# Kernel tuning notes

Measured on AMD Instinct MI355X. Metric: run time of the kernel, lower is better.

The kernel has to match this reference:

```python
import jax, jax.numpy as jnp
import numpy as np

N_AGENTS = 32
STATE_DIM = 6 * N_AGENTS      # 192
CONTROL_DIM = 3 * N_AGENTS    # 96
HIDDEN = 100
NEWTON_ITERS = 40

# Index maps from the cvxpy objective:
#   p[u_x_r]^T u[u_idx] + p[u_y_r]^T u[2*u_idx] + p[u_z_r]^T u[3*u_idx]
_u_idx = np.arange(N_AGENTS)
P_IDX = np.concatenate([3 * np.arange(1, N_AGENTS + 1),
                        4 * np.arange(1, N_AGENTS + 1),
                        5 * np.arange(1, N_AGENTS + 1)])
U_IDX = np.concatenate([_u_idx, 2 * _u_idx, 3 * _u_idx])


def _p_net(t, z, W1, b1, W2, b2, W3, b3):
    # DefaultPNet: MLP on concat([t, z]) with tanh hiddens (hidden_dim=100)
    x = jnp.concatenate([t, z], axis=-1)          # [B, 1+STATE_DIM]
    h = jnp.tanh(x @ W1 + b1)
    h = jnp.tanh(h @ W2 + b2)
    return h @ W3 + b3                            # [B, STATE_DIM]


def _solve_qp(q):
    # min_u q^T u + 0.5||u||^2 + 0.25||u||^4  (unconstrained, strictly convex)
    # Stationarity: q + (1+||u||^2) u = 0 => u = -q/(1+s), s = ||u||^2
    # => s (1+s)^2 = ||q||^2 ; solve scalar cubic per row via Newton.
    r = jnp.sum(q * q, axis=-1)                   # [B]
    s0 = jnp.cbrt(r)                              # good init: s ~ r^(1/3) for large r

    def step(s, _):
        one = 1.0 + s
        f = s * one * one - r
        fp = one * one + 2.0 * s * one
        return jnp.maximum(s - f / fp, 0.0), None

    s, _ = jax.lax.scan(step, s0, None, length=NEWTON_ITERS)
    return -q / (1.0 + s)[:, None]                # [B, CONTROL_DIM]


def setup_inputs() -> dict:
    key = jax.random.key(0)
    ks = jax.random.split(key, 8)
    B = 131072
    in_dim = 1 + STATE_DIM
    sc1 = 1.0 / np.sqrt(in_dim)
    sc2 = 1.0 / np.sqrt(HIDDEN)
    return {
        "z": jax.random.normal(ks[0], (B, STATE_DIM), jnp.float32),
        "t": jax.random.uniform(ks[1], (B, 1), jnp.float32),
        "W1": jax.random.normal(ks[2], (in_dim, HIDDEN), jnp.float32) * sc1,
        "b1": jnp.zeros((HIDDEN,), jnp.float32),
        "W2": jax.random.normal(ks[3], (HIDDEN, HIDDEN), jnp.float32) * sc2,
        "b2": jnp.zeros((HIDDEN,), jnp.float32),
        "W3": jax.random.normal(ks[4], (HIDDEN, STATE_DIM), jnp.float32) * sc2,
        "b3": jnp.zeros((STATE_DIM,), jnp.float32),
    }


def reference(z, t, W1, b1, W2, b2, W3, b3):
    p = _p_net(t, z, W1, b1, W2, b2, W3, b3)      # [B, STATE_DIM]
    # Accumulate linear coefficients onto u (indices overlap, so scatter-add)
    q = jnp.zeros((p.shape[0], CONTROL_DIM), p.dtype).at[:, U_IDX].add(p[:, P_IDX])
    return _solve_qp(q)                            # ustar [B, CONTROL_DIM]
```

## Files before the change

kernel.cpp:

```cpp
#include <hip/hip_runtime.h>
#include <hip/hip_bf16.h>


typedef __attribute__((ext_vector_type(8))) short short8;
typedef __attribute__((ext_vector_type(4))) float f32x4;

__device__ __forceinline__ unsigned short f2bf(float f) {
  unsigned u = __float_as_uint(f);
  u += 0x7fffu + ((u >> 16) & 1u);
  return (unsigned short)(u >> 16);
}
__device__ __forceinline__ float tanh_fast(float x) {
  float ax = fabsf(x);
  float e = __builtin_amdgcn_exp2f(ax * -2.88539008177792681f);
  float r = (1.f - e) * __builtin_amdgcn_rcpf(1.f + e);
  return copysignf(r, x);
}
__device__ __forceinline__ short8 pack_bf8(f32x4 a, f32x4 b) {
  union { short8 s; __hip_bfloat162 h[4]; } u;
  u.h[0] = __float22bfloat162_rn(make_float2(a[0], a[1]));
  u.h[1] = __float22bfloat162_rn(make_float2(a[2], a[3]));
  u.h[2] = __float22bfloat162_rn(make_float2(b[0], b[1]));
  u.h[3] = __float22bfloat162_rn(make_float2(b[2], b[3]));
  return u.s;
}
__device__ __forceinline__ unsigned pk2u(float lo, float hi) {
  union { __hip_bfloat162 h; unsigned u; } x;
  x.h = __float22bfloat162_rn(make_float2(lo, hi));
  return x.u;
}

__global__ void cvx_prep(const float* __restrict__ W1, const float* __restrict__ b1,
                         const float* __restrict__ W2, const float* __restrict__ b2,
                         const float* __restrict__ W3, const float* __restrict__ b3,
                         short* __restrict__ pw) {
  int idx = blockIdx.x * 256 + threadIdx.x;

  if (idx < 21504) {
    int kt = idx / 3584, rem = idx % 3584;
    int nt = rem / 512, e = rem % 512;
    int lane = e >> 3, j = e & 7;
    int k = kt * 32 + (lane >> 4) * 8 + j;
    int n = nt * 16 + (lane & 15);
    float wv = (n < 100) ? W1[(k + 1) * 100 + n] : 0.f;
    pw[(kt * 7 + nt) * 512 + e] = (short)f2bf(wv);
    return;
  }
  idx -= 21504;
  if (idx < 14336) {
    int kt = idx / 3584, rem = idx % 3584;
    int nt = rem / 512, e = rem % 512;
    int lane = e >> 3, j = e & 7;
    int k = kt * 32 + (lane >> 4) * 8 + j;
    int n = nt * 16 + (lane & 15);
    float wv = (k < 100 && n < 100) ? W2[k * 100 + n] : 0.f;
    pw[21504 + (kt * 7 + nt) * 512 + e] = (short)f2bf(wv);
    return;
  }
  idx -= 14336;
  if (idx < 12288) {
    int kt = idx / 3072, rem = idx % 3072;
    int nt = rem / 512, e = rem % 512;
    int lane = e >> 3, j = e & 7;
    int k = kt * 32 + (lane >> 4) * 8 + j;
    int u = nt * 16 + (lane & 15);
    float wv = 0.f;
    if (k < 100) {
      const float* wr = W3 + k * 192;
      if (u <= 31) wv += wr[3 * u + 3];
      if ((u & 1) == 0 && u <= 62) wv += wr[2 * u + 4];
      if (u % 3 == 0 && u <= 93) wv += wr[(5 * u) / 3 + 5];
    }
    pw[35840 + (kt * 6 + nt) * 512 + e] = (short)f2bf(wv);
    return;
  }
  idx -= 12288;
  float* cb = (float*)(pw + 48128);
  if (idx < 112) { cb[idx] = (idx < 100) ? W1[idx] : 0.f; return; }
  idx -= 112;
  if (idx < 112) { cb[112 + idx] = (idx < 100) ? b1[idx] : 0.f; return; }
  idx -= 112;
  if (idx < 112) { cb[224 + idx] = (idx < 100) ? b2[idx] : 0.f; return; }
  idx -= 112;
  if (idx < 96) {
    int u = idx;
    float v = 0.f;
    if (u <= 31) v += b3[3 * u + 3];
    if ((u & 1) == 0 && u <= 62) v += b3[2 * u + 4];
    if (u % 3 == 0 && u <= 93) v += b3[(5 * u) / 3 + 5];
    cb[336 + u] = v;
  }
}

__global__ __launch_bounds__(512, 2) void cvx_main(
    const float* __restrict__ zin, const float* __restrict__ tin,
    const short* __restrict__ pw, float* __restrict__ out) {
  __shared__ __align__(16) short wbuf[48128];
  __shared__ __align__(16) float cbl[448];

  const int tid = threadIdx.x;
  const int wid = tid >> 6;
  const int lane = tid & 63;
  const int l15 = lane & 15;
  const int qd = lane >> 4;
  const int lo_src = ((lane & 16) << 1) + l15;
  const int hi_src = lo_src + 16;
  const bool selA = lane < 32;

  for (int f = wid; f < 94; f += 8) {
    const short* g = pw + f * 512 + lane * 8;
    __builtin_amdgcn_global_load_lds(
        (const __attribute__((address_space(1))) void*)g,
        (__attribute__((address_space(3))) void*)&wbuf[f * 512], 16, 0, 0);
  }
  if (tid < 448) cbl[tid] = ((const float*)(pw + 48128))[tid];

  const int row0 = blockIdx.x * 512 + wid * 32;

  short8 XB[2][6];
  float tc0, tc1;
#pragma unroll
  for (int bt = 0; bt < 2; bt++) {
    const float* zr = zin + (size_t)(row0 + bt * 16 + l15) * 192 + qd * 8;
#pragma unroll
    for (int kt = 0; kt < 6; kt++) {
      f32x4 a = *(const f32x4*)(zr + kt * 32);
      f32x4 b = *(const f32x4*)(zr + kt * 32 + 4);
      XB[bt][kt] = pack_bf8(a, b);
    }
  }
  tc0 = tin[row0 + l15];
  tc1 = tin[row0 + 16 + l15];

  __syncthreads();

  auto buildHB = [&](const unsigned (&pkb)[7][2], int kt) -> short8 {
    union { short8 s; unsigned u[4]; } hb;
    if (kt < 3) {
      unsigned a0 = (unsigned)__shfl((int)pkb[2 * kt][0], lo_src);
      unsigned b0 = (unsigned)__shfl((int)pkb[2 * kt + 1][0], lo_src);
      unsigned a1 = (unsigned)__shfl((int)pkb[2 * kt][1], lo_src);
      unsigned b1_ = (unsigned)__shfl((int)pkb[2 * kt + 1][1], lo_src);
      unsigned a2 = (unsigned)__shfl((int)pkb[2 * kt][0], hi_src);
      unsigned b2_ = (unsigned)__shfl((int)pkb[2 * kt + 1][0], hi_src);
      unsigned a3 = (unsigned)__shfl((int)pkb[2 * kt][1], hi_src);
      unsigned b3_ = (unsigned)__shfl((int)pkb[2 * kt + 1][1], hi_src);
      hb.u[0] = selA ? a0 : b0;
      hb.u[1] = selA ? a1 : b1_;
      hb.u[2] = selA ? a2 : b2_;
      hb.u[3] = selA ? a3 : b3_;
    } else {
      hb.u[0] = (unsigned)__shfl((int)pkb[6][0], lo_src);
      hb.u[1] = (unsigned)__shfl((int)pkb[6][1], lo_src);
      hb.u[2] = (unsigned)__shfl((int)pkb[6][0], hi_src);
      hb.u[3] = (unsigned)__shfl((int)pkb[6][1], hi_src);
    }
    return hb.s;
  };

  short8 XN[2][6];
  float tn0, tn1;

#pragma unroll 1
  for (int ii = 0; ii < 2; ++ii) {
    const int rb = row0 + ii * 256;

    f32x4 acc[2][7];
#pragma unroll
    for (int nt = 0; nt < 7; nt++) {
      f32x4 zzz = {0.f, 0.f, 0.f, 0.f};
      acc[0][nt] = zzz; acc[1][nt] = zzz;
    }

    f32x4 sg[2][2][2];
    const float* zb = zin + (size_t)(row0 + 256 + l15) * 192 + qd * 8;

    if (ii == 0) {
#pragma unroll
      for (int bt = 0; bt < 2; bt++)
#pragma unroll
        for (int kp = 0; kp < 2; kp++) {
          sg[bt][kp][0] = *(const f32x4*)(zb + bt * 3072 + kp * 32);
          sg[bt][kp][1] = *(const f32x4*)(zb + bt * 3072 + kp * 32 + 4);
        }
      __builtin_amdgcn_sched_barrier(0);
    }

#pragma unroll
    for (int kt = 0; kt < 2; kt++)
#pragma unroll
      for (int nt = 0; nt < 7; nt++) {
        short8 wf = *(const short8*)&wbuf[(kt * 7 + nt) * 512 + lane * 8];
        acc[0][nt] = __builtin_amdgcn_mfma_f32_16x16x32_bf16(wf, XB[0][kt], acc[0][nt], 0, 0, 0);
        acc[1][nt] = __builtin_amdgcn_mfma_f32_16x16x32_bf16(wf, XB[1][kt], acc[1][nt], 0, 0, 0);
      }

    if (ii == 0) {
#pragma unroll
      for (int bt = 0; bt < 2; bt++)
#pragma unroll
        for (int kp = 0; kp < 2; kp++)
          XN[bt][kp] = pack_bf8(sg[bt][kp][0], sg[bt][kp][1]);
#pragma unroll
      for (int bt = 0; bt < 2; bt++)
#pragma unroll
        for (int kp = 0; kp < 2; kp++) {
          sg[bt][kp][0] = *(const f32x4*)(zb + bt * 3072 + (2 + kp) * 32);
          sg[bt][kp][1] = *(const f32x4*)(zb + bt * 3072 + (2 + kp) * 32 + 4);
        }
      __builtin_amdgcn_sched_barrier(0);
    }

#pragma unroll
    for (int kt = 2; kt < 4; kt++)
#pragma unroll
      for (int nt = 0; nt < 7; nt++) {
        short8 wf = *(const short8*)&wbuf[(kt * 7 + nt) * 512 + lane * 8];
        acc[0][nt] = __builtin_amdgcn_mfma_f32_16x16x32_bf16(wf, XB[0][kt], acc[0][nt], 0, 0, 0);
        acc[1][nt] = __builtin_amdgcn_mfma_f32_16x16x32_bf16(wf, XB[1][kt], acc[1][nt], 0, 0, 0);
      }

    if (ii == 0) {
#pragma unroll
      for (int bt = 0; bt < 2; bt++)
#pragma unroll
        for (int kp = 0; kp < 2; kp++)
          XN[bt][2 + kp] = pack_bf8(sg[bt][kp][0], sg[bt][kp][1]);
#pragma unroll
      for (int bt = 0; bt < 2; bt++)
#pragma unroll
        for (int kp = 0; kp < 2; kp++) {
          sg[bt][kp][0] = *(const f32x4*)(zb + bt * 3072 + (4 + kp) * 32);
          sg[bt][kp][1] = *(const f32x4*)(zb + bt * 3072 + (4 + kp) * 32 + 4);
        }
      tn0 = tin[row0 + 256 + l15];
      tn1 = tin[row0 + 256 + 16 + l15];
      __builtin_amdgcn_sched_barrier(0);
    }

#pragma unroll
    for (int kt = 4; kt < 6; kt++)
#pragma unroll
      for (int nt = 0; nt < 7; nt++) {
        short8 wf = *(const short8*)&wbuf[(kt * 7 + nt) * 512 + lane * 8];
        acc[0][nt] = __builtin_amdgcn_mfma_f32_16x16x32_bf16(wf, XB[0][kt], acc[0][nt], 0, 0, 0);
        acc[1][nt] = __builtin_amdgcn_mfma_f32_16x16x32_bf16(wf, XB[1][kt], acc[1][nt], 0, 0, 0);
      }

#pragma unroll
    for (int bt = 0; bt < 2; bt++) {
      float tcb = (bt == 0) ? tc0 : tc1;
#pragma unroll
      for (int nt = 0; nt < 7; nt++) {
        f32x4 w0v = *(const f32x4*)&cbl[nt * 16 + qd * 4];
        f32x4 b1v = *(const f32x4*)&cbl[112 + nt * 16 + qd * 4];
#pragma unroll
        for (int r = 0; r < 4; r++)
          acc[bt][nt][r] = tanh_fast(fmaf(tcb, w0v[r], acc[bt][nt][r] + b1v[r]));
      }
    }
    unsigned pk[2][7][2];
#pragma unroll
    for (int bt = 0; bt < 2; bt++)
#pragma unroll
      for (int nt = 0; nt < 7; nt++) {
        pk[bt][nt][0] = pk2u(acc[bt][nt][0], acc[bt][nt][1]);
        pk[bt][nt][1] = pk2u(acc[bt][nt][2], acc[bt][nt][3]);
      }

    if (ii == 0) {
#pragma unroll
      for (int bt = 0; bt < 2; bt++)
#pragma unroll
        for (int kp = 0; kp < 2; kp++)
          XN[bt][4 + kp] = pack_bf8(sg[bt][kp][0], sg[bt][kp][1]);
    }

#pragma unroll
    for (int nt = 0; nt < 7; nt++) {
      f32x4 zzz = {0.f, 0.f, 0.f, 0.f};
      acc[0][nt] = zzz; acc[1][nt] = zzz;
    }
#pragma unroll
    for (int kt = 0; kt < 4; kt++) {
      short8 hb0 = buildHB(pk[0], kt);
      short8 hb1 = buildHB(pk[1], kt);
#pragma unroll
      for (int nt = 0; nt < 7; nt++) {
        short8 wf = *(const short8*)&wbuf[(42 + kt * 7 + nt) * 512 + lane * 8];
        acc[0][nt] = __builtin_amdgcn_mfma_f32_16x16x32_bf16(wf, hb0, acc[0][nt], 0, 0, 0);
        acc[1][nt] = __builtin_amdgcn_mfma_f32_16x16x32_bf16(wf, hb1, acc[1][nt], 0, 0, 0);
      }
    }
#pragma unroll
    for (int bt = 0; bt < 2; bt++)
#pragma unroll
      for (int nt = 0; nt < 7; nt++) {
        f32x4 b2v = *(const f32x4*)&cbl[224 + nt * 16 + qd * 4];
#pragma unroll
        for (int r = 0; r < 4; r++)
          acc[bt][nt][r] = tanh_fast(acc[bt][nt][r] + b2v[r]);
        pk[bt][nt][0] = pk2u(acc[bt][nt][0], acc[bt][nt][1]);
        pk[bt][nt][1] = pk2u(acc[bt][nt][2], acc[bt][nt][3]);
      }

    f32x4 qa[2][6];
#pragma unroll
    for (int nt = 0; nt < 6; nt++) {
      f32x4 zzz = {0.f, 0.f, 0.f, 0.f};
      qa[0][nt] = zzz; qa[1][nt] = zzz;
    }
#pragma unroll
    for (int kt = 0; kt < 4; kt++) {
      short8 hb0 = buildHB(pk[0], kt);
      short8 hb1 = buildHB(pk[1], kt);
#pragma unroll
      for (int nt = 0; nt < 6; nt++) {
        short8 wf = *(const short8*)&wbuf[(70 + kt * 6 + nt) * 512 + lane * 8];
        qa[0][nt] = __builtin_amdgcn_mfma_f32_16x16x32_bf16(wf, hb0, qa[0][nt], 0, 0, 0);
        qa[1][nt] = __builtin_amdgcn_mfma_f32_16x16x32_bf16(wf, hb1, qa[1][nt], 0, 0, 0);
      }
    }

#pragma unroll
    for (int bt = 0; bt < 2; bt++) {
#pragma unroll
      for (int nt = 0; nt < 6; nt++) {
        f32x4 bqv = *(const f32x4*)&cbl[336 + nt * 16 + qd * 4];
        qa[bt][nt] += bqv;
      }
      float loc = 0.f;
#pragma unroll
      for (int nt = 0; nt < 6; nt++) {
        f32x4 q = qa[bt][nt];
        loc += q[0] * q[0] + q[1] * q[1] + q[2] * q[2] + q[3] * q[3];
      }
      loc += __shfl_xor(loc, 16);
      loc += __shfl_xor(loc, 32);
      float r2 = loc;
      float s = __builtin_amdgcn_exp2f(__builtin_amdgcn_logf(r2) * 0.333333333333f);
#pragma unroll
      for (int itn = 0; itn < 8; itn++) {
        float one = 1.f + s;
        float fv = fmaf(s * one, one, -r2);
        float fp = one * fmaf(2.f, s, one);
        s = fmaxf(s - fv * __builtin_amdgcn_rcpf(fp), 0.f);
      }
      float inv = -__builtin_amdgcn_rcpf(1.f + s);
      float* orow = out + (size_t)(rb + bt * 16 + l15) * 96;
#pragma unroll
      for (int nt = 0; nt < 6; nt++) {
        f32x4 v = qa[bt][nt] * inv;
        *(f32x4*)(orow + nt * 16 + qd * 4) = v;
      }
    }

    if (ii == 0) {
#pragma unroll
      for (int bt = 0; bt < 2; bt++)
#pragma unroll
        for (int kt = 0; kt < 6; kt++) XB[bt][kt] = XN[bt][kt];
      tc0 = tn0; tc1 = tn1;
    }
  }
}

extern "C" void kernel_launch(void* const* d_in, const int* in_sizes, int n_in,
                              void* d_out, int out_size, void* d_ws, size_t ws_size,
                              hipStream_t stream) {
  const float* z  = (const float*)d_in[0];
  const float* t  = (const float*)d_in[1];
  const float* W1 = (const float*)d_in[2];
  const float* b1 = (const float*)d_in[3];
  const float* W2 = (const float*)d_in[4];
  const float* b2 = (const float*)d_in[5];
  const float* W3 = (const float*)d_in[6];
  const float* b3 = (const float*)d_in[7];
  float* out = (float*)d_out;
  int B = in_sizes[0] / 192;

  short* pw = (short*)d_ws;
  cvx_prep<<<190, 256, 0, stream>>>(W1, b1, W2, b2, W3, b3, pw);
  cvx_main<<<B / 512, 512, 0, stream>>>(z, t, pw, out);
}
```

Baseline: 192.3 us.

## Process 64 rows per wave in one pass and simplify tanh

Each wave now handles four 16-row tiles (64 rows) in a single pass instead of two iterations of two tiles with software-prefetched next inputs. Every LDS weight fragment is reused across four MFMAs, which cuts LDS reads per row, and the manual prefetch pipeline is removed. Launch bounds drop to one block per SIMD group to make room for the larger register footprint, which lowers occupancy and latency hiding. tanh is rewritten as 1 - 2/(exp(2x)+1), dropping the abs/copysign ops but risking overflow handling for large inputs.

```diff
diff --git a/kernel.cpp b/kernel.cpp
--- a/kernel.cpp
+++ b/kernel.cpp
@@ -11,10 +11,8 @@
   return (unsigned short)(u >> 16);
 }
 __device__ __forceinline__ float tanh_fast(float x) {
-  float ax = fabsf(x);
-  float e = __builtin_amdgcn_exp2f(ax * -2.88539008177792681f);
-  float r = (1.f - e) * __builtin_amdgcn_rcpf(1.f + e);
-  return copysignf(r, x);
+  float e = __builtin_amdgcn_exp2f(x * 2.88539008177792681f);
+  return fmaf(-2.f, __builtin_amdgcn_rcpf(e + 1.f), 1.f);
 }
 __device__ __forceinline__ short8 pack_bf8(f32x4 a, f32x4 b) {
   union { short8 s; __hip_bfloat162 h[4]; } u;
@@ -92,7 +90,7 @@
   }
 }
 
-__global__ __launch_bounds__(512, 2) void cvx_main(
+__global__ __launch_bounds__(512, 1) void cvx_main(
     const float* __restrict__ zin, const float* __restrict__ tin,
     const short* __restrict__ pw, float* __restrict__ out) {
   __shared__ __align__(16) short wbuf[48128];
@@ -115,12 +113,12 @@
   }
   if (tid < 448) cbl[tid] = ((const float*)(pw + 48128))[tid];
 
-  const int row0 = blockIdx.x * 512 + wid * 32;
-
-  short8 XB[2][6];
-  float tc0, tc1;
-#pragma unroll
-  for (int bt = 0; bt < 2; bt++) {
+  const int row0 = blockIdx.x * 512 + wid * 64;
+
+  short8 XB[4][6];
+  float tc[4];
+#pragma unroll
+  for (int bt = 0; bt < 4; bt++) {
     const float* zr = zin + (size_t)(row0 + bt * 16 + l15) * 192 + qd * 8;
 #pragma unroll
     for (int kt = 0; kt < 6; kt++) {
@@ -128,9 +126,8 @@
       f32x4 b = *(const f32x4*)(zr + kt * 32 + 4);
       XB[bt][kt] = pack_bf8(a, b);
     }
-  }
-  tc0 = tin[row0 + l15];
-  tc1 = tin[row0 + 16 + l15];
+    tc[bt] = tin[row0 + bt * 16 + l15];
+  }
 
   __syncthreads();
 
@@ -158,209 +155,127 @@
     return hb.s;
   };
 
-  short8 XN[2][6];
-  float tn0, tn1;
-
-#pragma unroll 1
-  for (int ii = 0; ii < 2; ++ii) {
-    const int rb = row0 + ii * 256;
-
-    f32x4 acc[2][7];
+  f32x4 acc[4][7];
+#pragma unroll
+  for (int bt = 0; bt < 4; bt++)
 #pragma unroll
     for (int nt = 0; nt < 7; nt++) {
       f32x4 zzz = {0.f, 0.f, 0.f, 0.f};
-      acc[0][nt] = zzz; acc[1][nt] = zzz;
-    }
-
-    f32x4 sg[2][2][2];
-    const float* zb = zin + (size_t)(row0 + 256 + l15) * 192 + qd * 8;
-
-    if (ii == 0) {
-#pragma unroll
-      for (int bt = 0; bt < 2; bt++)
-#pragma unroll
-        for (int kp = 0; kp < 2; kp++) {
-          sg[bt][kp][0] = *(const f32x4*)(zb + bt * 3072 + kp * 32);
-          sg[bt][kp][1] = *(const f32x4*)(zb + bt * 3072 + kp * 32 + 4);
-        }
-      __builtin_amdgcn_sched_barrier(0);
-    }
-
-#pragma unroll
-    for (int kt = 0; kt < 2; kt++)
-#pragma unroll
-      for (int nt = 0; nt < 7; nt++) {
-        short8 wf = *(const short8*)&wbuf[(kt * 7 + nt) * 512 + lane * 8];
-        acc[0][nt] = __builtin_amdgcn_mfma_f32_16x16x32_bf16(wf, XB[0][kt], acc[0][nt], 0, 0, 0);
-        acc[1][nt] = __builtin_amdgcn_mfma_f32_16x16x32_bf16(wf, XB[1][kt], acc[1][nt], 0, 0, 0);
-      }
-
-    if (ii == 0) {
-#pragma unroll
-      for (int bt = 0; bt < 2; bt++)
-#pragma unroll
-        for (int kp = 0; kp < 2; kp++)
-          XN[bt][kp] = pack_bf8(sg[bt][kp][0], sg[bt][kp][1]);
-#pragma unroll
-      for (int bt = 0; bt < 2; bt++)
-#pragma unroll
-        for (int kp = 0; kp < 2; kp++) {
-          sg[bt][kp][0] = *(const f32x4*)(zb + bt * 3072 + (2 + kp) * 32);
-          sg[bt][kp][1] = *(const f32x4*)(zb + bt * 3072 + (2 + kp) * 32 + 4);
-        }
-      __builtin_amdgcn_sched_barrier(0);
-    }
-
-#pragma unroll
-    for (int kt = 2; kt < 4; kt++)
-#pragma unroll
-      for (int nt = 0; nt < 7; nt++) {
-        short8 wf = *(const short8*)&wbuf[(kt * 7 + nt) * 512 + lane * 8];
-        acc[0][nt] = __builtin_amdgcn_mfma_f32_16x16x32_bf16(wf, XB[0][kt], acc[0][nt], 0, 0, 0);
-        acc[1][nt] = __builtin_amdgcn_mfma_f32_16x16x32_bf16(wf, XB[1][kt], acc[1][nt], 0, 0, 0);
-      }
-
-    if (ii == 0) {
-#pragma unroll
-      for (int bt = 0; bt < 2; bt++)
-#pragma unroll
-        for (int kp = 0; kp < 2; kp++)
-          XN[bt][2 + kp] = pack_bf8(sg[bt][kp][0], sg[bt][kp][1]);
-#pragma unroll
-      for (int bt = 0; bt < 2; bt++)
-#pragma unroll
-        for (int kp = 0; kp < 2; kp++) {
-          sg[bt][kp][0] = *(const f32x4*)(zb + bt * 3072 + (4 + kp) * 32);
-          sg[bt][kp][1] = *(const f32x4*)(zb + bt * 3072 + (4 + kp) * 32 + 4);
-        }
-      tn0 = tin[row0 + 256 + l15];
-      tn1 = tin[row0 + 256 + 16 + l15];
-      __builtin_amdgcn_sched_barrier(0);
-    }
-
-#pragma unroll
-    for (int kt = 4; kt < 6; kt++)
-#pragma unroll
-      for (int nt = 0; nt < 7; nt++) {
-        short8 wf = *(const short8*)&wbuf[(kt * 7 + nt) * 512 + lane * 8];
-        acc[0][nt] = __builtin_amdgcn_mfma_f32_16x16x32_bf16(wf, XB[0][kt], acc[0][nt], 0, 0, 0);
-        acc[1][nt] = __builtin_amdgcn_mfma_f32_16x16x32_bf16(wf, XB[1][kt], acc[1][nt], 0, 0, 0);
-      }
-
-#pragma unroll
-    for (int bt = 0; bt < 2; bt++) {
-      float tcb = (bt == 0) ? tc0 : tc1;
-#pragma unroll
-      for (int nt = 0; nt < 7; nt++) {
-        f32x4 w0v = *(const f32x4*)&cbl[nt * 16 + qd * 4];
-        f32x4 b1v = *(const f32x4*)&cbl[112 + nt * 16 + qd * 4];
-#pragma unroll
-        for (int r = 0; r < 4; r++)
-          acc[bt][nt][r] = tanh_fast(fmaf(tcb, w0v[r], acc[bt][nt][r] + b1v[r]));
-      }
-    }
-    unsigned pk[2][7][2];
-#pragma unroll
-    for (int bt = 0; bt < 2; bt++)
-#pragma unroll
-      for (int nt = 0; nt < 7; nt++) {
-        pk[bt][nt][0] = pk2u(acc[bt][nt][0], acc[bt][nt][1]);
-        pk[bt][nt][1] = pk2u(acc[bt][nt][2], acc[bt][nt][3]);
-      }
-
-    if (ii == 0) {
-#pragma unroll
-      for (int bt = 0; bt < 2; bt++)
-#pragma unroll
-        for (int kp = 0; kp < 2; kp++)
-          XN[bt][4 + kp] = pack_bf8(sg[bt][kp][0], sg[bt][kp][1]);
-    }
-
+      acc[bt][nt] = zzz;
+    }
+#pragma unroll
+  for (int kt = 0; kt < 6; kt++)
+#pragma unroll
+    for (int nt = 0; nt < 7; nt++) {
+      short8 wf = *(const short8*)&wbuf[(kt * 7 + nt) * 512 + lane * 8];
+      acc[0][nt] = __builtin_amdgcn_mfma_f32_16x16x32_bf16(wf, XB[0][kt], acc[0][nt], 0, 0, 0);
+      acc[1][nt] = __builtin_amdgcn_mfma_f32_16x16x32_bf16(wf, XB[1][kt], acc[1][nt], 0, 0, 0);
+      acc[2][nt] = __builtin_amdgcn_mfma_f32_16x16x32_bf16(wf, XB[2][kt], acc[2][nt], 0, 0, 0);
+      acc[3][nt] = __builtin_amdgcn_mfma_f32_16x16x32_bf16(wf, XB[3][kt], acc[3][nt], 0, 0, 0);
+    }
+
+  unsigned pk[4][7][2];
+#pragma unroll
+  for (int bt = 0; bt < 4; bt++)
+#pragma unroll
+    for (int nt = 0; nt < 7; nt++) {
+      f32x4 w0v = *(const f32x4*)&cbl[nt * 16 + qd * 4];
+      f32x4 b1v = *(const f32x4*)&cbl[112 + nt * 16 + qd * 4];
+#pragma unroll
+      for (int r = 0; r < 4; r++)
+        acc[bt][nt][r] = tanh_fast(fmaf(tc[bt], w0v[r], acc[bt][nt][r] + b1v[r]));
+      pk[bt][nt][0] = pk2u(acc[bt][nt][0], acc[bt][nt][1]);
+      pk[bt][nt][1] = pk2u(acc[bt][nt][2], acc[bt][nt][3]);
+    }
+
+#pragma unroll
+  for (int bt = 0; bt < 4; bt++)
 #pragma unroll
     for (int nt = 0; nt < 7; nt++) {
       f32x4 zzz = {0.f, 0.f, 0.f, 0.f};
-      acc[0][nt] = zzz; acc[1][nt] = zzz;
-    }
-#pragma unroll
-    for (int kt = 0; kt < 4; kt++) {
-      short8 hb0 = buildHB(pk[0], kt);
-      short8 hb1 = buildHB(pk[1], kt);
-#pragma unroll
-      for (int nt = 0; nt < 7; nt++) {
-        short8 wf = *(const short8*)&wbuf[(42 + kt * 7 + nt) * 512 + lane * 8];
-        acc[0][nt] = __builtin_amdgcn_mfma_f32_16x16x32_bf16(wf, hb0, acc[0][nt], 0, 0, 0);
-        acc[1][nt] = __builtin_amdgcn_mfma_f32_16x16x32_bf16(wf, hb1, acc[1][nt], 0, 0, 0);
-      }
-    }
-#pragma unroll
-    for (int bt = 0; bt < 2; bt++)
-#pragma unroll
-      for (int nt = 0; nt < 7; nt++) {
-        f32x4 b2v = *(const f32x4*)&cbl[224 + nt * 16 + qd * 4];
-#pragma unroll
-        for (int r = 0; r < 4; r++)
-          acc[bt][nt][r] = tanh_fast(acc[bt][nt][r] + b2v[r]);
-        pk[bt][nt][0] = pk2u(acc[bt][nt][0], acc[bt][nt][1]);
-        pk[bt][nt][1] = pk2u(acc[bt][nt][2], acc[bt][nt][3]);
-      }
-
-    f32x4 qa[2][6];
+      acc[bt][nt] = zzz;
+    }
+#pragma unroll
+  for (int kt = 0; kt < 4; kt++) {
+    short8 hb0 = buildHB(pk[0], kt);
+    short8 hb1 = buildHB(pk[1], kt);
+    short8 hb2 = buildHB(pk[2], kt);
+    short8 hb3 = buildHB(pk[3], kt);
+#pragma unroll
+    for (int nt = 0; nt < 7; nt++) {
+      short8 wf = *(const short8*)&wbuf[(42 + kt * 7 + nt) * 512 + lane * 8];
+      acc[0][nt] = __builtin_amdgcn_mfma_f32_16x16x32_bf16(wf, hb0, acc[0][nt], 0, 0, 0);
+      acc[1][nt] = __builtin_amdgcn_mfma_f32_16x16x32_bf16(wf, hb1, acc[1][nt], 0, 0, 0);
+      acc[2][nt] = __builtin_amdgcn_mfma_f32_16x16x32_bf16(wf, hb2, acc[2][nt], 0, 0, 0);
+      acc[3][nt] = __builtin_amdgcn_mfma_f32_16x16x32_bf16(wf, hb3, acc[3][nt], 0, 0, 0);
+    }
+  }
+#pragma unroll
+  for (int bt = 0; bt < 4; bt++)
+#pragma unroll
+    for (int nt = 0; nt < 7; nt++) {
+      f32x4 b2v = *(const f32x4*)&cbl[224 + nt * 16 + qd * 4];
+#pragma unroll
+      for (int r = 0; r < 4; r++)
+        acc[bt][nt][r] = tanh_fast(acc[bt][nt][r] + b2v[r]);
+      pk[bt][nt][0] = pk2u(acc[bt][nt][0], acc[bt][nt][1]);
+      pk[bt][nt][1] = pk2u(acc[bt][nt][2], acc[bt][nt][3]);
+    }
+
+  f32x4 qa[4][6];
+#pragma unroll
+  for (int bt = 0; bt < 4; bt++)
 #pragma unroll
     for (int nt = 0; nt < 6; nt++) {
       f32x4 zzz = {0.f, 0.f, 0.f, 0.f};
-      qa[0][nt] = zzz; qa[1][nt] = zzz;
-    }
-#pragma unroll
-    for (int kt = 0; kt < 4; kt++) {
-      short8 hb0 = buildHB(pk[0], kt);
-      short8 hb1 = buildHB(pk[1], kt);
-#pragma unroll
-      for (int nt = 0; nt < 6; nt++) {
-        short8 wf = *(const short8*)&wbuf[(70 + kt * 6 + nt) * 512 + lane * 8];
-        qa[0][nt] = __builtin_amdgcn_mfma_f32_16x16x32_bf16(wf, hb0, qa[0][nt], 0, 0, 0);
-        qa[1][nt] = __builtin_amdgcn_mfma_f32_16x16x32_bf16(wf, hb1, qa[1][nt], 0, 0, 0);
-      }
-    }
-
-#pragma unroll
-    for (int bt = 0; bt < 2; bt++) {
-#pragma unroll
-      for (int nt = 0; nt < 6; nt++) {
-        f32x4 bqv = *(const f32x4*)&cbl[336 + nt * 16 + qd * 4];
-        qa[bt][nt] += bqv;
-      }
-      float loc = 0.f;
-#pragma unroll
-      for (int nt = 0; nt < 6; nt++) {
-        f32x4 q = qa[bt][nt];
-        loc += q[0] * q[0] + q[1] * q[1] + q[2] * q[2] + q[3] * q[3];
-      }
-      loc += __shfl_xor(loc, 16);
-      loc += __shfl_xor(loc, 32);
-      float r2 = loc;
-      float s = __builtin_amdgcn_exp2f(__builtin_amdgcn_logf(r2) * 0.333333333333f);
-#pragma unroll
-      for (int itn = 0; itn < 8; itn++) {
-        float one = 1.f + s;
-        float fv = fmaf(s * one, one, -r2);
-        float fp = one * fmaf(2.f, s, one);
-        s = fmaxf(s - fv * __builtin_amdgcn_rcpf(fp), 0.f);
-      }
-      float inv = -__builtin_amdgcn_rcpf(1.f + s);
-      float* orow = out + (size_t)(rb + bt * 16 + l15) * 96;
-#pragma unroll
-      for (int nt = 0; nt < 6; nt++) {
-        f32x4 v = qa[bt][nt] * inv;
-        *(f32x4*)(orow + nt * 16 + qd * 4) = v;
-      }
-    }
-
-    if (ii == 0) {
-#pragma unroll
-      for (int bt = 0; bt < 2; bt++)
-#pragma unroll
-        for (int kt = 0; kt < 6; kt++) XB[bt][kt] = XN[bt][kt];
-      tc0 = tn0; tc1 = tn1;
+      qa[bt][nt] = zzz;
+    }
+#pragma unroll
+  for (int kt = 0; kt < 4; kt++) {
+    short8 hb0 = buildHB(pk[0], kt);
+    short8 hb1 = buildHB(pk[1], kt);
+    short8 hb2 = buildHB(pk[2], kt);
+    short8 hb3 = buildHB(pk[3], kt);
+#pragma unroll
+    for (int nt = 0; nt < 6; nt++) {
+      short8 wf = *(const short8*)&wbuf[(70 + kt * 6 + nt) * 512 + lane * 8];
+      qa[0][nt] = __builtin_amdgcn_mfma_f32_16x16x32_bf16(wf, hb0, qa[0][nt], 0, 0, 0);
+      qa[1][nt] = __builtin_amdgcn_mfma_f32_16x16x32_bf16(wf, hb1, qa[1][nt], 0, 0, 0);
+      qa[2][nt] = __builtin_amdgcn_mfma_f32_16x16x32_bf16(wf, hb2, qa[2][nt], 0, 0, 0);
+      qa[3][nt] = __builtin_amdgcn_mfma_f32_16x16x32_bf16(wf, hb3, qa[3][nt], 0, 0, 0);
+    }
+  }
+
+#pragma unroll
+  for (int bt = 0; bt < 4; bt++) {
+#pragma unroll
+    for (int nt = 0; nt < 6; nt++) {
+      f32x4 bqv = *(const f32x4*)&cbl[336 + nt * 16 + qd * 4];
+      qa[bt][nt] += bqv;
+    }
+    float loc = 0.f;
+#pragma unroll
+    for (int nt = 0; nt < 6; nt++) {
+      f32x4 q = qa[bt][nt];
+      loc += q[0] * q[0] + q[1] * q[1] + q[2] * q[2] + q[3] * q[3];
+    }
+    loc += __shfl_xor(loc, 16);
+    loc += __shfl_xor(loc, 32);
+    float r2 = loc;
+    float s = __builtin_amdgcn_exp2f(__builtin_amdgcn_logf(r2) * 0.333333333333f);
+#pragma unroll
+    for (int itn = 0; itn < 8; itn++) {
+      float one = 1.f + s;
+      float fv = fmaf(s * one, one, -r2);
+      float fp = one * fmaf(2.f, s, one);
+      s = fmaxf(s - fv * __builtin_amdgcn_rcpf(fp), 0.f);
+    }
+    float inv = -__builtin_amdgcn_rcpf(1.f + s);
+    float* orow = out + (size_t)(row0 + bt * 16 + l15) * 96;
+#pragma unroll
+    for (int nt = 0; nt < 6; nt++) {
+      f32x4 v = qa[bt][nt] * inv;
+      *(f32x4*)(orow + nt * 16 + qd * 4) = v;
     }
   }
 }
```

After: 193.4 us. Within noise of the previous version (+0.6%).
